# Kernel tuning notes

Measured on AMD Instinct MI355X. Metric: run time of the kernel, lower is better.

Reference implementation:

```python
import jax, jax.numpy as jnp
import numpy as np

B, S, HID = 1, 2048, 4096
NH, NKV, D = 32, 8, 128          # query heads, kv heads, head_dim
GROUPS = NH // NKV               # GQA repeat factor = 4
WINDOW = 1024                    # sliding-window size
ROPE_BASE = 10000.0


def setup_inputs() -> dict:
    key = jax.random.key(0)
    k = jax.random.split(key, 5)
    hidden_states = jax.random.normal(k[0], (B, S, HID), jnp.float32)
    Wq = jax.random.normal(k[1], (HID, HID), jnp.float32) * 0.02
    Wk = jax.random.normal(k[2], (NKV * D, HID), jnp.float32) * 0.02
    Wv = jax.random.normal(k[3], (NKV * D, HID), jnp.float32) * 0.02
    Wo = jax.random.normal(k[4], (HID, HID), jnp.float32) * 0.02
    position_ids = jnp.arange(S, dtype=jnp.int64 if jax.config.jax_enable_x64 else jnp.int32)[None, :]
    # Sliding-window causal additive mask [B,1,S,S]: key j visible to query i iff i-WINDOW < j <= i
    i = jnp.arange(S)
    visible = (i[None, :] <= i[:, None]) & (i[:, None] - i[None, :] < WINDOW)
    neg = jnp.finfo(jnp.float32).min
    attention_mask = jnp.where(visible, 0.0, neg)[None, None, :, :].astype(jnp.float32)
    return {"hidden_states": hidden_states, "attention_mask": attention_mask,
            "position_ids": position_ids, "Wq": Wq, "Wk": Wk, "Wv": Wv, "Wo": Wo}


def _rotate_half(x):
    x1, x2 = x[..., : D // 2], x[..., D // 2:]
    return jnp.concatenate((-x2, x1), axis=-1)


def _rope_cos_sin(position_ids, dtype):
    # inv_freq over even dims; gather-by-position_ids == direct indexing
    inv_freq = 1.0 / (ROPE_BASE ** (jnp.arange(0, D, 2, dtype=jnp.float32) / D))  # [D/2]
    freqs = position_ids.astype(jnp.float32)[..., None] * inv_freq                # [B,S,D/2]
    emb = jnp.concatenate((freqs, freqs), axis=-1)                                # [B,S,D]
    cos = jnp.cos(emb)[:, None, :, :].astype(dtype)                               # [B,1,S,D]
    sin = jnp.sin(emb)[:, None, :, :].astype(dtype)
    return cos, sin


def reference(hidden_states, attention_mask, position_ids, Wq, Wk, Wv, Wo):
    bsz, q_len, _ = hidden_states.shape
    # projections (nn.Linear: y = x @ W.T)
    q = (hidden_states @ Wq.T).reshape(bsz, q_len, NH, D).transpose(0, 2, 1, 3)    # [B,NH,S,D]
    k = (hidden_states @ Wk.T).reshape(bsz, q_len, NKV, D).transpose(0, 2, 1, 3)   # [B,NKV,S,D]
    v = (hidden_states @ Wv.T).reshape(bsz, q_len, NKV, D).transpose(0, 2, 1, 3)
    cos, sin = _rope_cos_sin(position_ids, q.dtype)
    q = q * cos + _rotate_half(q) * sin
    k = k * cos + _rotate_half(k) * sin
    # GQA repeat_kv (repeat_interleave along head dim)
    k = jnp.repeat(k, GROUPS, axis=1)                                              # [B,NH,S,D]
    v = jnp.repeat(v, GROUPS, axis=1)
    scores = jnp.einsum('bhqd,bhkd->bhqk', q, k) / np.sqrt(D)                       # [B,NH,S,S]
    scores = scores + attention_mask
    scores = jnp.maximum(scores, jnp.finfo(scores.dtype).min)
    probs = jax.nn.softmax(scores.astype(jnp.float32), axis=-1).astype(q.dtype)
    out = jnp.einsum('bhqk,bhkd->bhqd', probs, v)                                   # [B,NH,S,D]
    out = out.transpose(0, 2, 1, 3).reshape(bsz, q_len, HID)
    return out @ Wo.T
```

## Files before the change

### kernel.cpp

```cpp
#include <hip/hip_runtime.h>

#define S_LEN 2048
#define HID   4096
#define NH    32
#define NKV   8
#define DH    128
#define KVD   (NKV*DH)
#define WIN   1024
#define NTOT  6144

typedef __bf16 bf16_t;
typedef __bf16 bfrag  __attribute__((ext_vector_type(8)));
typedef __bf16 bf4    __attribute__((ext_vector_type(4)));
typedef float  ffrag  __attribute__((ext_vector_type(4)));
typedef float  facc   __attribute__((ext_vector_type(16)));

__global__ __launch_bounds__(256) void cvt_h_kernel(const float* __restrict__ h,
                                                    bf16_t* __restrict__ hB) {
  int i = blockIdx.x * 256 + threadIdx.x;
  ffrag v = *(const ffrag*)(h + (size_t)i * 4);
  bf4 o;
  o[0] = (bf16_t)v[0]; o[1] = (bf16_t)v[1]; o[2] = (bf16_t)v[2]; o[3] = (bf16_t)v[3];
  *(bf4*)(hB + (size_t)i * 4) = o;
}

__global__ __launch_bounds__(256) void rope_table_kernel(float2* __restrict__ tab) {
  int i = blockIdx.x * 256 + threadIdx.x;
  int s = i >> 6, d = i & 63;
  float inv = exp2f((float)d * (-13.287712379549449f / 64.f));
  float ang = (float)s * inv;
  tab[i] = make_float2(cosf(ang), sinf(ang));
}

__device__ __forceinline__ void load_lds16(const bf16_t* g, bf16_t* l) {
  __builtin_amdgcn_global_load_lds((__attribute__((address_space(1))) void*)g,
                                   (__attribute__((address_space(3))) void*)l,
                                   16, 0, 0);
}

#define BARW() asm volatile("s_barrier" ::: "memory")
#define WAITV(n) asm volatile("s_waitcnt vmcnt(" #n ")" ::: "memory")
#define LGKM0() do { asm volatile("s_waitcnt lgkmcnt(0)" ::: "memory"); \
                     __builtin_amdgcn_sched_barrier(0); } while (0)

__device__ __forceinline__ bfrag cvt8(const float4& a, const float4& b) {
  bfrag w;
  w[0] = (bf16_t)a.x; w[1] = (bf16_t)a.y; w[2] = (bf16_t)a.z; w[3] = (bf16_t)a.w;
  w[4] = (bf16_t)b.x; w[5] = (bf16_t)b.y; w[6] = (bf16_t)b.z; w[7] = (bf16_t)b.w;
  return w;
}

__global__ __launch_bounds__(512, 4) void gemm_qkv_kernel(const bf16_t* __restrict__ hB,
                                                          const float* __restrict__ Wq,
                                                          const float* __restrict__ Wk,
                                                          const float* __restrict__ Wv,
                                                          bf16_t* __restrict__ C) {
  constexpr int K     = 4096;
  constexpr int NT    = K / 64;
  constexpr int ABUFE = 128 * 64;
  constexpr int BBUFE = 192 * 64;
  __shared__ __align__(16) bf16_t lds[2 * ABUFE + 2 * BBUFE];
  bf16_t* As0 = lds;
  bf16_t* Bs0 = lds + 2 * ABUFE;

  const int raw  = blockIdx.x;
  const int xcd  = raw & 7;
  const int slot = raw >> 3;
  const int bx   = xcd * 4 + (slot & 3);
  const int by   = slot >> 2;
  const int row0 = by * 128;
  const int col0 = bx * 192;

  const int tid  = threadIdx.x;
  const int wave = tid >> 6;
  const int lane = tid & 63;
  const int wr = wave >> 2, wc = wave & 3;
  const int n = lane & 15, qd = lane >> 4;

  const int rsub = tid >> 3;
  const int gA   = (tid & 7) ^ (rsub & 7);
  const bf16_t* Ag = hB + (size_t)(row0 + rsub) * K + gA * 8;
  const int wbase = wave * 512;

  const int gB   = tid & 7;
  const float* Bgf0; const float* Bgf1; const float* Bgf2;
  {
    int r0_ = col0 + rsub;
    Bgf0 = (r0_ < HID) ? (Wq + (size_t)r0_ * K)
         : (r0_ < HID + KVD) ? (Wk + (size_t)(r0_ - HID) * K)
                             : (Wv + (size_t)(r0_ - HID - KVD) * K);
    int r1_ = col0 + rsub + 64;
    Bgf1 = (r1_ < HID) ? (Wq + (size_t)r1_ * K)
         : (r1_ < HID + KVD) ? (Wk + (size_t)(r1_ - HID) * K)
                             : (Wv + (size_t)(r1_ - HID - KVD) * K);
    int r2_ = col0 + rsub + 128;
    Bgf2 = (r2_ < HID) ? (Wq + (size_t)r2_ * K)
         : (r2_ < HID + KVD) ? (Wk + (size_t)(r2_ - HID) * K)
                             : (Wv + (size_t)(r2_ - HID - KVD) * K);
  }
  const int bwoff = rsub * 64 + ((gB ^ (rsub & 7)) * 8);

  const int pg0 = ( qd      ^ (n & 7)) * 8;
  const int pg1 = ((4 | qd) ^ (n & 7)) * 8;
  const int abase = (wr * 64 + n) * 64;
  const int bbase = (wc * 48 + n) * 64;

  ffrag acc[4][3];
#pragma unroll
  for (int mt = 0; mt < 4; ++mt)
#pragma unroll
    for (int nt = 0; nt < 3; ++nt) {
      acc[mt][nt][0] = 0.f; acc[mt][nt][1] = 0.f; acc[mt][nt][2] = 0.f; acc[mt][nt][3] = 0.f;
    }

  float4 bb00, bb01, bb10, bb11, bb20, bb21;

#define QKV_LOADB(t) do { const int ko_ = (t) * 64 + gB * 8;            \
    bb00 = *(const float4*)(Bgf0 + ko_); bb01 = *(const float4*)(Bgf0 + ko_ + 4); \
    bb10 = *(const float4*)(Bgf1 + ko_); bb11 = *(const float4*)(Bgf1 + ko_ + 4); \
    bb20 = *(const float4*)(Bgf2 + ko_); bb21 = *(const float4*)(Bgf2 + ko_ + 4); } while (0)
#define QKV_WRITEB(s) do { bf16_t* bs_ = Bs0 + (s) * BBUFE;             \
    *(bfrag*)&bs_[bwoff]        = cvt8(bb00, bb01);                     \
    *(bfrag*)&bs_[4096 + bwoff] = cvt8(bb10, bb11);                     \
    *(bfrag*)&bs_[8192 + bwoff] = cvt8(bb20, bb21); } while (0)

  auto STAGE_A = [&](int t, int s) {
    const int ko = t * 64;
    bf16_t* as = As0 + s * ABUFE + wbase;
    load_lds16(Ag + ko, as);
    load_lds16(Ag + (size_t)64 * K + ko, as + 4096);
  };

  STAGE_A(0, 0); QKV_LOADB(0);
  WAITV(0);
  QKV_WRITEB(0);
  STAGE_A(1, 1); QKV_LOADB(1);
  LGKM0();
  BARW();

  for (int t = 0; t < NT; ++t) {
    const int s = t & 1;
    const bf16_t* Asl = As0 + s * ABUFE;
    const bf16_t* Bsl = Bs0 + s * BBUFE;
    bfrag av[4], bv[3];

#pragma unroll
    for (int mt = 0; mt < 4; ++mt) av[mt] = *(const bfrag*)(Asl + abase + mt * 1024 + pg0);
#pragma unroll
    for (int nt = 0; nt < 3; ++nt) bv[nt] = *(const bfrag*)(Bsl + bbase + nt * 1024 + pg0);
    __builtin_amdgcn_s_setprio(1);
#pragma unroll
    for (int mt = 0; mt < 4; ++mt)
#pragma unroll
      for (int nt = 0; nt < 3; ++nt)
        acc[mt][nt] = __builtin_amdgcn_mfma_f32_16x16x32_bf16(av[mt], bv[nt], acc[mt][nt], 0, 0, 0);
    __builtin_amdgcn_s_setprio(0);

#pragma unroll
    for (int mt = 0; mt < 4; ++mt) av[mt] = *(const bfrag*)(Asl + abase + mt * 1024 + pg1);
#pragma unroll
    for (int nt = 0; nt < 3; ++nt) bv[nt] = *(const bfrag*)(Bsl + bbase + nt * 1024 + pg1);
    __builtin_amdgcn_s_setprio(1);
#pragma unroll
    for (int mt = 0; mt < 4; ++mt)
#pragma unroll
      for (int nt = 0; nt < 3; ++nt)
        acc[mt][nt] = __builtin_amdgcn_mfma_f32_16x16x32_bf16(av[mt], bv[nt], acc[mt][nt], 0, 0, 0);
    __builtin_amdgcn_s_setprio(0);

    LGKM0();
    BARW();
    if (t + 2 < NT) STAGE_A(t + 2, s);
    if (t + 1 < NT) {
      if (t + 2 < NT) { WAITV(2); } else { WAITV(0); }
      QKV_WRITEB(s ^ 1);
      if (t + 2 < NT) QKV_LOADB(t + 2);
      LGKM0();
      BARW();
    }
  }

  const int orow = row0 + wr * 64 + qd * 4;
  const int ocol = col0 + wc * 48 + n;
#pragma unroll
  for (int mt = 0; mt < 4; ++mt)
#pragma unroll
    for (int nt = 0; nt < 3; ++nt)
#pragma unroll
      for (int r = 0; r < 4; ++r)
        C[(size_t)(orow + mt * 16 + r) * NTOT + (ocol + nt * 16)] = (bf16_t)acc[mt][nt][r];
#undef QKV_LOADB
#undef QKV_WRITEB
}

__global__ __launch_bounds__(256, 2) void gemm_out_kernel(const bf16_t* __restrict__ A,
                                                          const float* __restrict__ Wo,
                                                          float* __restrict__ out) {
  constexpr int K     = 4096;
  constexpr int NT    = K / 64;
  constexpr int ABUFE = 128 * 64;
  constexpr int BBUFE = 128 * 64;
  __shared__ __align__(16) bf16_t lds[2 * ABUFE + 2 * BBUFE];
  bf16_t* As0 = lds;
  bf16_t* Bs0 = lds + 2 * ABUFE;

  const int raw  = blockIdx.x;
  const int xcd  = raw & 7;
  const int slot = raw >> 3;
  const int bx   = xcd * 4 + (slot & 3);
  const int by   = slot >> 2;
  const int row0 = by * 128;
  const int col0 = bx * 128;

  const int tid  = threadIdx.x;
  const int wave = tid >> 6;
  const int lane = tid & 63;
  const int wm = wave >> 1, wn = wave & 1;
  const int l31 = lane & 31, hi = lane >> 5, l7 = lane & 7;

  const int rsub = tid >> 3;
  const int gA   = (tid & 7) ^ (rsub & 7);
  const bf16_t* Ag = A + (size_t)(row0 + rsub) * K + gA * 8;
  const int wbase = wave * 512;

  const int gB = tid & 7;
  const float* Bgf = Wo + (size_t)(col0 + rsub) * K;
  const int bwoff = rsub * 64 + ((gB ^ (rsub & 7)) * 8);

  int pgk[4];
#pragma unroll
  for (int ks = 0; ks < 4; ++ks) pgk[ks] = ((ks * 2 + hi) ^ l7) * 8;
  const int aoff = (wm * 64 + l31) * 64;
  const int boff = (wn * 64 + l31) * 64;

  facc acc[2][2];
#pragma unroll
  for (int mt = 0; mt < 2; ++mt)
#pragma unroll
    for (int nt = 0; nt < 2; ++nt)
#pragma unroll
      for (int j = 0; j < 16; ++j) acc[mt][nt][j] = 0.f;

  float4 bb00, bb01, bb10, bb11, bb20, bb21, bb30, bb31;

#define OUT_LOADB(t) do { const int ko_ = (t) * 64 + gB * 8;                        \
    bb00 = *(const float4*)(Bgf + ko_);                                             \
    bb01 = *(const float4*)(Bgf + ko_ + 4);                                         \
    bb10 = *(const float4*)(Bgf + (size_t)32 * K + ko_);                            \
    bb11 = *(const float4*)(Bgf + (size_t)32 * K + ko_ + 4);                        \
    bb20 = *(const float4*)(Bgf + (size_t)64 * K + ko_);                            \
    bb21 = *(const float4*)(Bgf + (size_t)64 * K + ko_ + 4);                        \
    bb30 = *(const float4*)(Bgf + (size_t)96 * K + ko_);                            \
    bb31 = *(const float4*)(Bgf + (size_t)96 * K + ko_ + 4); } while (0)
#define OUT_WRITEB(s) do { bf16_t* bs_ = Bs0 + (s) * BBUFE;                         \
    *(bfrag*)&bs_[bwoff]        = cvt8(bb00, bb01);                                 \
    *(bfrag*)&bs_[2048 + bwoff] = cvt8(bb10, bb11);                                 \
    *(bfrag*)&bs_[4096 + bwoff] = cvt8(bb20, bb21);                                 \
    *(bfrag*)&bs_[6144 + bwoff] = cvt8(bb30, bb31); } while (0)

  auto STAGE_A = [&](int t, int s) {
    const int ko = t * 64;
    bf16_t* as = As0 + s * ABUFE + wbase;
#pragma unroll
    for (int i = 0; i < 4; ++i)
      load_lds16(Ag + (size_t)(i * 32) * K + ko, as + i * 2048);
  };

  STAGE_A(0, 0); OUT_LOADB(0);
  WAITV(0);
  OUT_WRITEB(0);
  STAGE_A(1, 1); OUT_LOADB(1);
  LGKM0();
  BARW();

  for (int t = 0; t < NT; ++t) {
    const int s = t & 1;
    const bf16_t* Asl = As0 + s * ABUFE;
    const bf16_t* Bsl = Bs0 + s * BBUFE;

#pragma unroll
    for (int ks = 0; ks < 4; ++ks) {
      bfrag av0 = *(const bfrag*)(Asl + aoff + pgk[ks]);
      bfrag av1 = *(const bfrag*)(Asl + aoff + 2048 + pgk[ks]);
      bfrag bv0 = *(const bfrag*)(Bsl + boff + pgk[ks]);
      bfrag bv1 = *(const bfrag*)(Bsl + boff + 2048 + pgk[ks]);
      __builtin_amdgcn_s_setprio(1);
      acc[0][0] = __builtin_amdgcn_mfma_f32_32x32x16_bf16(av0, bv0, acc[0][0], 0, 0, 0);
      acc[0][1] = __builtin_amdgcn_mfma_f32_32x32x16_bf16(av0, bv1, acc[0][1], 0, 0, 0);
      acc[1][0] = __builtin_amdgcn_mfma_f32_32x32x16_bf16(av1, bv0, acc[1][0], 0, 0, 0);
      acc[1][1] = __builtin_amdgcn_mfma_f32_32x32x16_bf16(av1, bv1, acc[1][1], 0, 0, 0);
      __builtin_amdgcn_s_setprio(0);
    }

    LGKM0();
    BARW();
    if (t + 2 < NT) STAGE_A(t + 2, s);
    if (t + 1 < NT) {
      if (t + 2 < NT) { WAITV(4); } else { WAITV(0); }
      OUT_WRITEB(s ^ 1);
      if (t + 2 < NT) OUT_LOADB(t + 2);
      LGKM0();
      BARW();
    }
  }

  const int orow = row0 + wm * 64 + 4 * hi;
  const int ocol = col0 + wn * 64 + l31;
#pragma unroll
  for (int mt = 0; mt < 2; ++mt)
#pragma unroll
    for (int nt = 0; nt < 2; ++nt)
#pragma unroll
      for (int j = 0; j < 16; ++j) {
        int r = orow + mt * 32 + (j & 3) + 8 * (j >> 2);
        out[(size_t)r * HID + (ocol + nt * 32)] = acc[mt][nt][j];
      }
#undef OUT_LOADB
#undef OUT_WRITEB
}

__global__ __launch_bounds__(256) void ropecvt_kernel(const bf16_t* __restrict__ Cqkv,
                                                      const float2* __restrict__ tab,
                                                      bf16_t* __restrict__ Qb,
                                                      bf16_t* __restrict__ Kb,
                                                      bf16_t* __restrict__ Vb) {
  int idx = blockIdx.x * 256 + threadIdx.x;
  int g  = idx & 7;
  int t  = idx >> 3;
  int hh = t % 48;
  int s  = t / 48;
  const bf16_t* r0 = Cqkv + (size_t)s * NTOT + hh * 128;
  bfrag a0 = *(const bfrag*)&r0[g * 8];
  bfrag a1 = *(const bfrag*)&r0[g * 8 + 64];
  bf16_t* p;
  bool rope;
  if (hh < NH)           { p = Qb + (size_t)s * HID + hh * DH;        rope = true; }
  else if (hh < NH+NKV)  { p = Kb + (size_t)s * KVD + (hh - NH) * DH; rope = true; }
  else                   { p = Vb + (size_t)s * KVD + (hh - 40) * DH; rope = false; }
  bfrag o1, o2;
  if (rope) {
    const float2* tb = tab + s * 64 + g * 8;
#pragma unroll
    for (int j = 0; j < 8; ++j) {
      float x1 = (float)a0[j];
      float x2 = (float)a1[j];
      float2 cs = tb[j];
      o1[j] = (bf16_t)(x1 * cs.x - x2 * cs.y);
      o2[j] = (bf16_t)(x2 * cs.x + x1 * cs.y);
    }
  } else {
#pragma unroll
    for (int j = 0; j < 8; ++j) { o1[j] = a0[j]; o2[j] = a1[j]; }
  }
  *(bfrag*)&p[g * 8]      = o1;
  *(bfrag*)&p[g * 8 + 64] = o2;
}

#define KS_STRIDE 136
#define VT_STRIDE 72
#define PS_STRIDE 72

__global__ __launch_bounds__(256, 3) void attn_kernel(const bf16_t* __restrict__ Q,
                                                      const bf16_t* __restrict__ Kc,
                                                      const bf16_t* __restrict__ Vc,
                                                      bf16_t* __restrict__ AO) {
  const int qt   = 31 - blockIdx.x;
  const int h    = blockIdx.y;
  const int kvh  = h >> 2;
  const int q0   = qt * 64;
  const int tid  = threadIdx.x;
  const int wq   = tid >> 6;
  const int lane = tid & 63;
  const int n    = lane & 15;
  const int quad = lane >> 4;
  const float scale = 0.08838834764831845f;

  __shared__ __align__(16) bf16_t Ks[64 * KS_STRIDE];
  __shared__ __align__(16) bf16_t VT[128 * VT_STRIDE];
  __shared__ __align__(16) bf16_t Ps[4][16 * PS_STRIDE];

  bfrag aq[4];
#pragma unroll
  for (int kc = 0; kc < 4; ++kc) {
    bfrag t = *(const bfrag*)&Q[(size_t)(q0 + wq * 16 + n) * HID + h * DH + kc * 32 + quad * 8];
#pragma unroll
    for (int e = 0; e < 8; ++e) t[e] = (bf16_t)((float)t[e] * scale);
    aq[kc] = t;
  }

  ffrag acc[8];
#pragma unroll
  for (int dt = 0; dt < 8; ++dt) { acc[dt][0] = 0.f; acc[dt][1] = 0.f; acc[dt][2] = 0.f; acc[dt][3] = 0.f; }
  float lrow[4] = {0.f, 0.f, 0.f, 0.f};

  const int ktlo = (q0 >= WIN) ? ((q0 - (WIN - 1)) >> 6) : 0;
  const int kthi = (q0 + 63) >> 6;

  const int kg = tid & 15;
  const int dg = tid >> 4;

  bfrag pk[4], pv[4];
  {
    const int k0 = ktlo * 64;
#pragma unroll
    for (int i = 0; i < 4; ++i) {
      int pos = i * 256 + tid;
      pk[i] = *(const bfrag*)&Kc[(size_t)(k0 + (pos >> 4)) * KVD + kvh * DH + (pos & 15) * 8];
    }
#pragma unroll
    for (int j = 0; j < 4; ++j)
      pv[j] = *(const bfrag*)&Vc[(size_t)(k0 + j * 16 + kg) * KVD + kvh * DH + dg * 8];
  }

  for (int kt = ktlo; kt <= kthi; ++kt) {
    const int k0 = kt * 64;
    __syncthreads();
#pragma unroll
    for (int i = 0; i < 4; ++i) {
      int pos = i * 256 + tid;
      *(bfrag*)&Ks[(pos >> 4) * KS_STRIDE + (pos & 15) * 8] = pk[i];
    }
#pragma unroll
    for (int i = 0; i < 8; ++i) {
      bf4 pkk;
      pkk[0] = pv[0][i]; pkk[1] = pv[1][i]; pkk[2] = pv[2][i]; pkk[3] = pv[3][i];
      *(bf4*)&VT[(dg * 8 + i) * VT_STRIDE + kg * 4] = pkk;
    }
    __syncthreads();
    if (kt < kthi) {
      const int k1 = k0 + 64;
#pragma unroll
      for (int i = 0; i < 4; ++i) {
        int pos = i * 256 + tid;
        pk[i] = *(const bfrag*)&Kc[(size_t)(k1 + (pos >> 4)) * KVD + kvh * DH + (pos & 15) * 8];
      }
#pragma unroll
      for (int j = 0; j < 4; ++j)
        pv[j] = *(const bfrag*)&Vc[(size_t)(k1 + j * 16 + kg) * KVD + kvh * DH + dg * 8];
    }

    ffrag s[4];
#pragma unroll
    for (int nt = 0; nt < 4; ++nt) { s[nt][0] = 0.f; s[nt][1] = 0.f; s[nt][2] = 0.f; s[nt][3] = 0.f; }
#pragma unroll
    for (int kc = 0; kc < 4; ++kc) {
      bfrag bk[4];
#pragma unroll
      for (int nt = 0; nt < 4; ++nt)
        bk[nt] = *(const bfrag*)&Ks[(nt * 16 + n) * KS_STRIDE + kc * 32 + quad * 8];
      __builtin_amdgcn_s_setprio(1);
#pragma unroll
      for (int nt = 0; nt < 4; ++nt)
        s[nt] = __builtin_amdgcn_mfma_f32_16x16x32_bf16(aq[kc], bk[nt], s[nt], 0, 0, 0);
      __builtin_amdgcn_s_setprio(0);
    }

    const bool full = (k0 + 63 <= q0) && (q0 + 63 - k0 < WIN);
    if (!full) {
#pragma unroll
      for (int nt = 0; nt < 4; ++nt)
#pragma unroll
        for (int r = 0; r < 4; ++r) {
          int q = q0 + wq * 16 + quad * 4 + r;
          int k = k0 + nt * 16 + n;
          bool vis = (k <= q) && ((q - k) < WIN);
          if (!vis) s[nt][r] = -1e30f;
        }
    }

#pragma unroll
    for (int r = 0; r < 4; ++r) {
      bf4 pkk;
      float ps0 = __expf(s[0][r]);
      float ps1 = __expf(s[1][r]);
      float ps2 = __expf(s[2][r]);
      float ps3 = __expf(s[3][r]);
      lrow[r] += (ps0 + ps1) + (ps2 + ps3);
      pkk[0] = (bf16_t)ps0; pkk[1] = (bf16_t)ps1; pkk[2] = (bf16_t)ps2; pkk[3] = (bf16_t)ps3;
      *(bf4*)&Ps[wq][(quad * 4 + r) * PS_STRIDE + n * 4] = pkk;
    }

#pragma unroll
    for (int kc = 0; kc < 2; ++kc) {
      bfrag ap = *(const bfrag*)&Ps[wq][n * PS_STRIDE + kc * 32 + quad * 8];
#pragma unroll
      for (int dt = 0; dt < 8; dt += 4) {
        bfrag bv0 = *(const bfrag*)&VT[((dt + 0) * 16 + n) * VT_STRIDE + kc * 32 + quad * 8];
        bfrag bv1 = *(const bfrag*)&VT[((dt + 1) * 16 + n) * VT_STRIDE + kc * 32 + quad * 8];
        bfrag bv2 = *(const bfrag*)&VT[((dt + 2) * 16 + n) * VT_STRIDE + kc * 32 + quad * 8];
        bfrag bv3 = *(const bfrag*)&VT[((dt + 3) * 16 + n) * VT_STRIDE + kc * 32 + quad * 8];
        __builtin_amdgcn_s_setprio(1);
        acc[dt + 0] = __builtin_amdgcn_mfma_f32_16x16x32_bf16(ap, bv0, acc[dt + 0], 0, 0, 0);
        acc[dt + 1] = __builtin_amdgcn_mfma_f32_16x16x32_bf16(ap, bv1, acc[dt + 1], 0, 0, 0);
        acc[dt + 2] = __builtin_amdgcn_mfma_f32_16x16x32_bf16(ap, bv2, acc[dt + 2], 0, 0, 0);
        acc[dt + 3] = __builtin_amdgcn_mfma_f32_16x16x32_bf16(ap, bv3, acc[dt + 3], 0, 0, 0);
        __builtin_amdgcn_s_setprio(0);
      }
    }
  }

#pragma unroll
  for (int off = 1; off < 16; off <<= 1)
#pragma unroll
    for (int r = 0; r < 4; ++r) lrow[r] += __shfl_xor(lrow[r], off);
  float inv[4];
#pragma unroll
  for (int r = 0; r < 4; ++r) inv[r] = 1.f / lrow[r];
#pragma unroll
  for (int dt = 0; dt < 8; ++dt)
#pragma unroll
    for (int r = 0; r < 4; ++r)
      AO[(size_t)(q0 + wq * 16 + quad * 4 + r) * HID + h * DH + dt * 16 + n] =
          (bf16_t)(acc[dt][r] * inv[r]);
}

extern "C" void kernel_launch(void* const* d_in, const int* in_sizes, int n_in,
                              void* d_out, int out_size, void* d_ws, size_t ws_size,
                              hipStream_t stream) {
  const float* h  = (const float*)d_in[0];
  const float* Wq = (const float*)d_in[3];
  const float* Wk = (const float*)d_in[4];
  const float* Wv = (const float*)d_in[5];
  const float* Wo = (const float*)d_in[6];
  float* out = (float*)d_out;

  char* ws = (char*)d_ws;
  const size_t MB = (size_t)1 << 20;
  bf16_t* hB    = (bf16_t*)(ws + 0 * MB);
  bf16_t* Qb    = (bf16_t*)(ws + 0 * MB);
  bf16_t* Cqkv  = (bf16_t*)(ws + 64 * MB);
  float2* Rtab  = (float2*)(ws + 88 * MB);
  bf16_t* AOb   = (bf16_t*)(ws + 96 * MB);
  bf16_t* Kb    = (bf16_t*)(ws + 112 * MB);
  bf16_t* Vb    = (bf16_t*)(ws + 116 * MB);

  rope_table_kernel<<<(S_LEN * 64) / 256, 256, 0, stream>>>(Rtab);

  cvt_h_kernel<<<(S_LEN * HID / 4) / 256, 256, 0, stream>>>(h, hB);

  gemm_qkv_kernel<<<512, 512, 0, stream>>>(hB, Wq, Wk, Wv, Cqkv);

  ropecvt_kernel<<<(S_LEN * 48 * 8) / 256, 256, 0, stream>>>(Cqkv, Rtab, Qb, Kb, Vb);

  attn_kernel<<<dim3(32, NH), 256, 0, stream>>>(Qb, Kb, Vb, AOb);

  gemm_out_kernel<<<512, 256, 0, stream>>>(AOb, Wo, out);
}
```

Before: 504.2 us.

## Pre-convert QKV weights to bf16 and stage B tiles via direct LDS loads

```diff
diff --git a/kernel.cpp b/kernel.cpp
--- a/kernel.cpp
+++ b/kernel.cpp
@@ -15,13 +15,23 @@
 typedef float  ffrag  __attribute__((ext_vector_type(4)));
 typedef float  facc   __attribute__((ext_vector_type(16)));
 
-__global__ __launch_bounds__(256) void cvt_h_kernel(const float* __restrict__ h,
-                                                    bf16_t* __restrict__ hB) {
+__global__ __launch_bounds__(256) void cvt4_kernel(const float* __restrict__ h,
+    const float* __restrict__ Wq, const float* __restrict__ Wk, const float* __restrict__ Wv,
+    bf16_t* __restrict__ hB, bf16_t* __restrict__ WqB,
+    bf16_t* __restrict__ WkB, bf16_t* __restrict__ WvB) {
   int i = blockIdx.x * 256 + threadIdx.x;
-  ffrag v = *(const ffrag*)(h + (size_t)i * 4);
+  const int N0 = S_LEN * HID / 4;
+  const int N1 = N0 + HID * HID / 4;
+  const int N2 = N1 + KVD * HID / 4;
+  const float* s; bf16_t* d; int off;
+  if (i < N0)      { s = h;  d = hB;  off = i; }
+  else if (i < N1) { s = Wq; d = WqB; off = i - N0; }
+  else if (i < N2) { s = Wk; d = WkB; off = i - N1; }
+  else             { s = Wv; d = WvB; off = i - N2; }
+  ffrag v = *(const ffrag*)(s + (size_t)off * 4);
   bf4 o;
   o[0] = (bf16_t)v[0]; o[1] = (bf16_t)v[1]; o[2] = (bf16_t)v[2]; o[3] = (bf16_t)v[3];
-  *(bf4*)(hB + (size_t)i * 4) = o;
+  *(bf4*)(d + (size_t)off * 4) = o;
 }
 
 __global__ __launch_bounds__(256) void rope_table_kernel(float2* __restrict__ tab) {
@@ -51,9 +61,7 @@
 }
 
 __global__ __launch_bounds__(512, 4) void gemm_qkv_kernel(const bf16_t* __restrict__ hB,
-                                                          const float* __restrict__ Wq,
-                                                          const float* __restrict__ Wk,
-                                                          const float* __restrict__ Wv,
+                                                          const bf16_t* __restrict__ Wqkv,
                                                           bf16_t* __restrict__ C) {
   constexpr int K     = 4096;
   constexpr int NT    = K / 64;
@@ -78,27 +86,10 @@
   const int n = lane & 15, qd = lane >> 4;
 
   const int rsub = tid >> 3;
-  const int gA   = (tid & 7) ^ (rsub & 7);
-  const bf16_t* Ag = hB + (size_t)(row0 + rsub) * K + gA * 8;
+  const int sg   = (tid & 7) ^ (rsub & 7);
+  const bf16_t* Ag = hB   + (size_t)(row0 + rsub) * K + sg * 8;
+  const bf16_t* Bg = Wqkv + (size_t)(col0 + rsub) * K + sg * 8;
   const int wbase = wave * 512;
-
-  const int gB   = tid & 7;
-  const float* Bgf0; const float* Bgf1; const float* Bgf2;
-  {
-    int r0_ = col0 + rsub;
-    Bgf0 = (r0_ < HID) ? (Wq + (size_t)r0_ * K)
-         : (r0_ < HID + KVD) ? (Wk + (size_t)(r0_ - HID) * K)
-                             : (Wv + (size_t)(r0_ - HID - KVD) * K);
-    int r1_ = col0 + rsub + 64;
-    Bgf1 = (r1_ < HID) ? (Wq + (size_t)r1_ * K)
-         : (r1_ < HID + KVD) ? (Wk + (size_t)(r1_ - HID) * K)
-                             : (Wv + (size_t)(r1_ - HID - KVD) * K);
-    int r2_ = col0 + rsub + 128;
-    Bgf2 = (r2_ < HID) ? (Wq + (size_t)r2_ * K)
-         : (r2_ < HID + KVD) ? (Wk + (size_t)(r2_ - HID) * K)
-                             : (Wv + (size_t)(r2_ - HID - KVD) * K);
-  }
-  const int bwoff = rsub * 64 + ((gB ^ (rsub & 7)) * 8);
 
   const int pg0 = ( qd      ^ (n & 7)) * 8;
   const int pg1 = ((4 | qd) ^ (n & 7)) * 8;
@@ -113,29 +104,19 @@
       acc[mt][nt][0] = 0.f; acc[mt][nt][1] = 0.f; acc[mt][nt][2] = 0.f; acc[mt][nt][3] = 0.f;
     }
 
-  float4 bb00, bb01, bb10, bb11, bb20, bb21;
-
-#define QKV_LOADB(t) do { const int ko_ = (t) * 64 + gB * 8;            \
-    bb00 = *(const float4*)(Bgf0 + ko_); bb01 = *(const float4*)(Bgf0 + ko_ + 4); \
-    bb10 = *(const float4*)(Bgf1 + ko_); bb11 = *(const float4*)(Bgf1 + ko_ + 4); \
-    bb20 = *(const float4*)(Bgf2 + ko_); bb21 = *(const float4*)(Bgf2 + ko_ + 4); } while (0)
-#define QKV_WRITEB(s) do { bf16_t* bs_ = Bs0 + (s) * BBUFE;             \
-    *(bfrag*)&bs_[bwoff]        = cvt8(bb00, bb01);                     \
-    *(bfrag*)&bs_[4096 + bwoff] = cvt8(bb10, bb11);                     \
-    *(bfrag*)&bs_[8192 + bwoff] = cvt8(bb20, bb21); } while (0)
-
-  auto STAGE_A = [&](int t, int s) {
+  auto STAGE = [&](int t, int s) {
     const int ko = t * 64;
     bf16_t* as = As0 + s * ABUFE + wbase;
+    bf16_t* bs = Bs0 + s * BBUFE + wbase;
     load_lds16(Ag + ko, as);
     load_lds16(Ag + (size_t)64 * K + ko, as + 4096);
+    load_lds16(Bg + ko, bs);
+    load_lds16(Bg + (size_t)64 * K + ko, bs + 4096);
+    load_lds16(Bg + (size_t)128 * K + ko, bs + 8192);
   };
 
-  STAGE_A(0, 0); QKV_LOADB(0);
-  WAITV(0);
-  QKV_WRITEB(0);
-  STAGE_A(1, 1); QKV_LOADB(1);
-  LGKM0();
+  STAGE(0, 0); STAGE(1, 1);
+  WAITV(5);
   BARW();
 
   for (int t = 0; t < NT; ++t) {
@@ -170,12 +151,9 @@
 
     LGKM0();
     BARW();
-    if (t + 2 < NT) STAGE_A(t + 2, s);
+    if (t + 2 < NT) STAGE(t + 2, s);
     if (t + 1 < NT) {
-      if (t + 2 < NT) { WAITV(2); } else { WAITV(0); }
-      QKV_WRITEB(s ^ 1);
-      if (t + 2 < NT) QKV_LOADB(t + 2);
-      LGKM0();
+      if (t + 2 < NT) { WAITV(5); } else { WAITV(0); }
       BARW();
     }
   }
@@ -189,8 +167,6 @@
 #pragma unroll
       for (int r = 0; r < 4; ++r)
         C[(size_t)(orow + mt * 16 + r) * NTOT + (ocol + nt * 16)] = (bf16_t)acc[mt][nt][r];
-#undef QKV_LOADB
-#undef QKV_WRITEB
 }
 
 __global__ __launch_bounds__(256, 2) void gemm_out_kernel(const bf16_t* __restrict__ A,
@@ -528,6 +504,9 @@
   const size_t MB = (size_t)1 << 20;
   bf16_t* hB    = (bf16_t*)(ws + 0 * MB);
   bf16_t* Qb    = (bf16_t*)(ws + 0 * MB);
+  bf16_t* WqB   = (bf16_t*)(ws + 16 * MB);
+  bf16_t* WkB   = (bf16_t*)(ws + 48 * MB);
+  bf16_t* WvB   = (bf16_t*)(ws + 56 * MB);
   bf16_t* Cqkv  = (bf16_t*)(ws + 64 * MB);
   float2* Rtab  = (float2*)(ws + 88 * MB);
   bf16_t* AOb   = (bf16_t*)(ws + 96 * MB);
@@ -536,9 +515,10 @@
 
   rope_table_kernel<<<(S_LEN * 64) / 256, 256, 0, stream>>>(Rtab);
 
-  cvt_h_kernel<<<(S_LEN * HID / 4) / 256, 256, 0, stream>>>(h, hB);
-
-  gemm_qkv_kernel<<<512, 512, 0, stream>>>(hB, Wq, Wk, Wv, Cqkv);
+  cvt4_kernel<<<(S_LEN * HID + HID * HID + 2 * KVD * HID) / 4 / 256, 256, 0, stream>>>(
+      h, Wq, Wk, Wv, hB, WqB, WkB, WvB);
+
+  gemm_qkv_kernel<<<512, 512, 0, stream>>>(hB, WqB, Cqkv);
 
   ropecvt_kernel<<<(S_LEN * 48 * 8) / 256, 256, 0, stream>>>(Cqkv, Rtab, Qb, Kb, Vb);
 
```

Result: faster. 468.7 us (-7.0%).
